# Optimization experiments

Measured on AMD Instinct MI355X. Metric: run time of the kernel, lower is better.

Reference implementation:

```python
import jax, jax.numpy as jnp
import numpy as np

N = 50000
E = 800000
IN_DIM = 128
HID = 128
OUT = 4
EPS = 1e-5


def setup_inputs() -> dict:
    key = jax.random.key(0)
    ks = jax.random.split(key, 16)
    glorot = lambda k, i, o: jax.random.uniform(k, (i, o), jnp.float32, -1.0, 1.0) * jnp.sqrt(6.0 / (i + o))
    return {
        "x": jax.random.normal(ks[0], (N, IN_DIM), jnp.float32),
        "edge_index": jax.random.randint(ks[1], (2, E), 0, N, jnp.int64),
        # SAGEConv layer 0: lin_l (aggregated neighbors, with bias), lin_r (self, no bias)
        "W_l0": glorot(ks[2], IN_DIM, HID), "b_l0": jnp.zeros((HID,), jnp.float32),
        "W_r0": glorot(ks[3], IN_DIM, HID),
        # SAGEConv layer 1
        "W_l1": glorot(ks[4], HID, HID), "b_l1": jnp.zeros((HID,), jnp.float32),
        "W_r1": glorot(ks[5], HID, HID),
        # LayerNorms
        "g0": jnp.ones((HID,), jnp.float32), "beta0": jnp.zeros((HID,), jnp.float32),
        "g1": jnp.ones((HID,), jnp.float32), "beta1": jnp.zeros((HID,), jnp.float32),
        # head
        "W_h": glorot(ks[6], HID, OUT), "b_h": jnp.zeros((OUT,), jnp.float32),
    }


def _sage_conv(x, src, dst, deg_inv, W_l, b_l, W_r):
    # mean-aggregate source features at destination nodes, then project
    agg = jax.ops.segment_sum(x[src], dst, num_segments=N) * deg_inv  # [N, d]
    return agg @ W_l + b_l + x @ W_r


def _layer_norm(x, g, b):
    mu = jnp.mean(x, axis=-1, keepdims=True)
    var = jnp.mean(jnp.square(x - mu), axis=-1, keepdims=True)
    return (x - mu) * jax.lax.rsqrt(var + EPS) * g + b


def reference(x, edge_index, W_l0, b_l0, W_r0, W_l1, b_l1, W_r1, g0, beta0, g1, beta1, W_h, b_h):
    src, dst = edge_index[0], edge_index[1]
    deg = jax.ops.segment_sum(jnp.ones((E,), jnp.float32), dst, num_segments=N)
    deg_inv = (1.0 / jnp.maximum(deg, 1.0))[:, None]  # mean over empty neighborhood -> 0

    h = _sage_conv(x, src, dst, deg_inv, W_l0, b_l0, W_r0)
    h = jax.nn.relu(_layer_norm(h, g0, beta0))
    h = _sage_conv(h, src, dst, deg_inv, W_l1, b_l1, W_r1)
    h = jax.nn.relu(_layer_norm(h, g1, beta1))
    return h @ W_h + b_h  # [N, 4]
```

## Files before the change

### kernel.cpp

```cpp
#include <hip/hip_runtime.h>

#define NN 50000
#define EE 800000
#define DIM 128
#define KK 256
#define OUTD 4
#define EPSV 1e-5f
#define OTS 132
#define NB 196
#define SLOT 8192
#define ACHUNK 4096
#define NA 196

using short8v = __attribute__((ext_vector_type(8))) short;
using f32x4v  = __attribute__((ext_vector_type(4))) float;

__device__ __forceinline__ unsigned short f2bf(float f) {
    union { float f; unsigned u; } x; x.f = f;
    unsigned r = x.u + 0x7FFF + ((x.u >> 16) & 1);
    return (unsigned short)(r >> 16);
}
__device__ __forceinline__ float bf2f(unsigned short u) {
    union { unsigned u; float f; } x; x.u = ((unsigned)u) << 16;
    return x.f;
}


#define XB_BLK 6250
#define W_BLK  256
__global__ __launch_bounds__(256) void prepA_kernel(
    const float* __restrict__ x, ushort* __restrict__ xqb,
    const float* __restrict__ Wl0, const float* __restrict__ Wr0,
    const float* __restrict__ Wl1, const float* __restrict__ Wr1,
    ushort* __restrict__ Wt0, ushort* __restrict__ Wt1,
    const int* __restrict__ src, const int* __restrict__ dst,
    int* __restrict__ bucketCursor, unsigned* __restrict__ pairs)
{
    int b = blockIdx.x;
    int tid = threadIdx.x;
    if (b < XB_BLK) {
        int i = b * 256 + tid;
        float4 v = ((const float4*)x)[i];
        ushort4 o;
        o.x = f2bf(v.x); o.y = f2bf(v.y); o.z = f2bf(v.z); o.w = f2bf(v.w);
        int node = i >> 5;
        int k = (i * 4) & 127;
        int p = k >> 5, off = k & 31;
        *(ushort4*)(xqb + ((size_t)p * NN + node) * 32 + off) = o;
        return;
    }
    if (b < XB_BLK + W_BLK) {
        int idx = (b - XB_BLK) * 256 + tid;
        int which = idx >> 15;
        int j = (idx >> 8) & 127;
        int k = idx & 255;
        const float* Wl = which ? Wl1 : Wl0;
        const float* Wr = which ? Wr1 : Wr0;
        ushort* Wt = which ? Wt1 : Wt0;
        float v = (k < 128) ? Wl[k * DIM + j] : Wr[(k - 128) * DIM + j];
        Wt[j * KK + k] = f2bf(v);
        return;
    }

    __shared__ int hist[256];
    __shared__ int scanb[256];
    __shared__ int exStart[256];
    __shared__ int cur2[256];
    __shared__ int gBase[256];
    __shared__ unsigned stage[ACHUNK];
    int ab = b - XB_BLK - W_BLK;
    int eBase = ab * ACHUNK;
    int total = min(ACHUNK, EE - eBase);

    hist[tid] = 0;
    __syncthreads();

    #pragma unroll
    for (int i = 0; i < 16; i++) {
        int idx = i * 256 + tid;
        if (idx < total) {
            int d = dst[eBase + idx];
            atomicAdd(&hist[d >> 8], 1);
        }
    }
    __syncthreads();
    int cntv = hist[tid];
    scanb[tid] = cntv;
    __syncthreads();
    #pragma unroll
    for (int off = 1; off < 256; off <<= 1) {
        int add = (tid >= off) ? scanb[tid - off] : 0;
        __syncthreads();
        scanb[tid] += add;
        __syncthreads();
    }
    int ex = scanb[tid] - cntv;
    exStart[tid] = ex;
    cur2[tid] = ex;
    if (tid < NB) gBase[tid] = (cntv > 0) ? atomicAdd(&bucketCursor[tid], cntv) : 0;
    __syncthreads();

    #pragma unroll
    for (int i = 0; i < 16; i++) {
        int idx = i * 256 + tid;
        if (idx < total) {
            int e = eBase + idx;
            int d = dst[e], s = src[e];
            int bb = d >> 8;
            int sp = atomicAdd(&cur2[bb], 1);
            stage[sp] = ((unsigned)d << 16) | (unsigned)s;
        }
    }
    __syncthreads();

    #pragma unroll
    for (int i = 0; i < 16; i++) {
        int idx = i * 256 + tid;
        if (idx < total) {
            unsigned v = stage[idx];
            int bb = v >> 24;
            int pos = gBase[bb] + (idx - exStart[bb]);
            if (pos < SLOT) pairs[(size_t)bb * SLOT + pos] = v;
        }
    }
}

__global__ __launch_bounds__(256) void passB_kernel(
    const int* __restrict__ bucketCursor,
    const unsigned* __restrict__ pairs,
    int* __restrict__ rowptr, ushort* __restrict__ colS)
{
    __shared__ int bscan[256];
    __shared__ int cw[256];
    __shared__ int pre2[256];
    __shared__ unsigned val_lds[SLOT];
    int tid = threadIdx.x;
    int b = blockIdx.x;

    int c = (tid < NB) ? min(bucketCursor[tid], SLOT) : 0;
    bscan[tid] = c;
    __syncthreads();
    #pragma unroll
    for (int off = 1; off < 256; off <<= 1) {
        int add = (tid >= off) ? bscan[tid - off] : 0;
        __syncthreads();
        bscan[tid] += add;
        __syncthreads();
    }
    int myBase = b ? bscan[b - 1] : 0;
    int count  = bscan[b] - myBase;
    __syncthreads();

    cw[tid] = 0;
    __syncthreads();

    const unsigned* pb = pairs + (size_t)b * SLOT;
    for (int p = tid; p < count; p += 256) {
        unsigned v = pb[p];
        val_lds[p] = v;
        atomicAdd(&cw[(v >> 16) & 255], 1);
    }
    __syncthreads();
    int cnode = cw[tid];
    bscan[tid] = cnode;
    __syncthreads();
    #pragma unroll
    for (int off = 1; off < 256; off <<= 1) {
        int add = (tid >= off) ? bscan[tid - off] : 0;
        __syncthreads();
        bscan[tid] += add;
        __syncthreads();
    }
    int preEx = bscan[tid] - cnode;
    pre2[tid] = preEx;
    int nodeBase = b << 8;
    if (nodeBase + tid < NN) rowptr[nodeBase + tid] = myBase + preEx;
    if (b == NB - 1 && tid == 0) rowptr[NN] = myBase + count;
    cw[tid] = 0;
    __syncthreads();

    for (int p = tid; p < count; p += 256) {
        unsigned v = val_lds[p];
        int dl = (v >> 16) & 255;
        int r = atomicAdd(&cw[dl], 1);
        colS[myBase + pre2[dl] + r] = (ushort)(v & 0xFFFF);
    }
}

template <int DO_HEAD>
__global__ __launch_bounds__(256) void sage_fused_kernel(
    const ushort* __restrict__ featG,
    const int* __restrict__ rowptr, const ushort* __restrict__ colS,
    const ushort* __restrict__ WtB,
    const float* __restrict__ bl,
    const float* __restrict__ g, const float* __restrict__ beta,
    const float* __restrict__ Wh, const float* __restrict__ bh,
    void* __restrict__ outp)
{
    __shared__ __align__(16) char smem[32 * OTS * 4];
    __shared__ float mu_s[32], ri_s[32];
    ushort* featB = (ushort*)smem;
    float*  oT    = (float*)smem;
    #define OT(n, k) oT[(n) * OTS + (k)]

    int tid = threadIdx.x;
    int base = blockIdx.x * 32;
    int lane = tid & 63, w = tid >> 6;

    #pragma unroll
    for (int i = 0; i < 2; i++) {
        int idx = tid + i * 256;
        int n = idx >> 4, c = idx & 15;
        int node = base + n;
        short8v xv = {};
        if (node < NN) {
            int p = c >> 2;
            int off = (c & 3) * 8;
            xv = *(const short8v*)(featG + ((size_t)p * NN + node) * 32 + off);
        }
        int kb = (256 + c * 16) ^ ((n & 7) << 4);
        *(short8v*)(featB + n * KK + (kb >> 1)) = xv;
    }

    {
        int n = tid >> 3;
        int sub = tid & 7;
        int node = base + n;
        int beg = 0, end = 0;
        if (node < NN) { beg = rowptr[node]; end = rowptr[node + 1]; }
        float di = 1.0f / fmaxf((float)(end - beg), 1.0f);
        #pragma unroll 1
        for (int p = 0; p < 4; p++) {
            const ushort* xq = featG + (size_t)p * NN * 32 + sub * 4;
            float a0[4], a1[4], a2[4], a3[4];
            #pragma unroll
            for (int j = 0; j < 4; j++) { a0[j] = 0.f; a1[j] = 0.f; a2[j] = 0.f; a3[j] = 0.f; }
            int e = beg;
            for (; e + 3 < end; e += 4) {
                int s0 = colS[e], s1 = colS[e + 1], s2 = colS[e + 2], s3 = colS[e + 3];
                ushort4 v0 = *(const ushort4*)(xq + s0 * 32);
                ushort4 v1 = *(const ushort4*)(xq + s1 * 32);
                ushort4 v2 = *(const ushort4*)(xq + s2 * 32);
                ushort4 v3 = *(const ushort4*)(xq + s3 * 32);
                a0[0] += bf2f(v0.x); a0[1] += bf2f(v0.y); a0[2] += bf2f(v0.z); a0[3] += bf2f(v0.w);
                a1[0] += bf2f(v1.x); a1[1] += bf2f(v1.y); a1[2] += bf2f(v1.z); a1[3] += bf2f(v1.w);
                a2[0] += bf2f(v2.x); a2[1] += bf2f(v2.y); a2[2] += bf2f(v2.z); a2[3] += bf2f(v2.w);
                a3[0] += bf2f(v3.x); a3[1] += bf2f(v3.y); a3[2] += bf2f(v3.z); a3[3] += bf2f(v3.w);
            }
            for (; e < end; e++) {
                int s0 = colS[e];
                ushort4 v0 = *(const ushort4*)(xq + s0 * 32);
                a0[0] += bf2f(v0.x); a0[1] += bf2f(v0.y); a0[2] += bf2f(v0.z); a0[3] += bf2f(v0.w);
            }
            ushort4 o;
            float r0 = (a0[0] + a1[0] + a2[0] + a3[0]) * di;
            float r1 = (a0[1] + a1[1] + a2[1] + a3[1]) * di;
            float r2 = (a0[2] + a1[2] + a2[2] + a3[2]) * di;
            float r3 = (a0[3] + a1[3] + a2[3] + a3[3]) * di;
            o.x = f2bf(r0); o.y = f2bf(r1); o.z = f2bf(r2); o.w = f2bf(r3);
            int kb = (p * 64 + sub * 8) ^ ((n & 7) << 4);
            *(ushort4*)(featB + n * KK + (kb >> 1)) = o;
        }
    }
    __syncthreads();

    int l15 = lane & 15, q = lane >> 4;
    f32x4v acc00 = {}, acc01 = {}, acc10 = {}, acc11 = {};
    const ushort* wbase = WtB + (size_t)(w * 32) * KK;
    int n0 = l15, n1 = 16 + l15;
    int sw = (l15 & 7) << 4;
    #pragma unroll
    for (int ks = 0; ks < 8; ks++) {
        int kbA = ks * 64 + q * 16;
        short8v a0 = *(const short8v*)(featB + n0 * KK + (((kbA) ^ sw) >> 1));
        short8v a1 = *(const short8v*)(featB + n1 * KK + (((kbA) ^ sw) >> 1));
        int koff = ks * 32 + q * 8;
        short8v b0 = *(const short8v*)(wbase + (size_t)l15 * KK + koff);
        short8v b1 = *(const short8v*)(wbase + (size_t)(16 + l15) * KK + koff);
        acc00 = __builtin_amdgcn_mfma_f32_16x16x32_bf16(a0, b0, acc00, 0, 0, 0);
        acc01 = __builtin_amdgcn_mfma_f32_16x16x32_bf16(a0, b1, acc01, 0, 0, 0);
        acc10 = __builtin_amdgcn_mfma_f32_16x16x32_bf16(a1, b0, acc10, 0, 0, 0);
        acc11 = __builtin_amdgcn_mfma_f32_16x16x32_bf16(a1, b1, acc11, 0, 0, 0);
    }
    __syncthreads();

    {
        int c0 = w * 32 + l15, c1 = c0 + 16;
        float bl0v = bl[c0], bl1v = bl[c1];
        #pragma unroll
        for (int r = 0; r < 4; r++) {
            int r0 = q * 4 + r, r1 = 16 + q * 4 + r;
            OT(r0, c0) = acc00[r] + bl0v;
            OT(r0, c1) = acc01[r] + bl1v;
            OT(r1, c0) = acc10[r] + bl0v;
            OT(r1, c1) = acc11[r] + bl1v;
        }
    }
    __syncthreads();

    {
        int n = tid >> 3, l = tid & 7;
        float s = 0.f, s2 = 0.f;
        #pragma unroll
        for (int kk = 0; kk < 16; kk++) {
            float v = OT(n, l * 16 + kk);
            s += v; s2 += v * v;
        }
        #pragma unroll
        for (int off = 4; off; off >>= 1) {
            s  += __shfl_down(s, off, 8);
            s2 += __shfl_down(s2, off, 8);
        }
        if (l == 0) {
            float mu = s * (1.0f / DIM);
            float var = s2 * (1.0f / DIM) - mu * mu;
            mu_s[n] = mu;
            ri_s[n] = rsqrtf(fmaxf(var, 0.f) + EPSV);
        }
    }
    __syncthreads();

    if (!DO_HEAD) {
        ushort* hout = (ushort*)outp;
        #pragma unroll
        for (int i = 0; i < 16; i++) {
            int idx = tid + i * 256;
            int n = idx >> 7, k = idx & 127;
            int node = base + n;
            if (node < NN) {
                float v = (OT(n, k) - mu_s[n]) * ri_s[n] * g[k] + beta[k];
                hout[((size_t)(k >> 5) * NN + node) * 32 + (k & 31)] = f2bf(fmaxf(v, 0.f));
            }
        }
    } else {
        float* fout = (float*)outp;
        float vals[16];
        #pragma unroll
        for (int i = 0; i < 16; i++) {
            int idx = tid + i * 256;
            int n = idx >> 7, k = idx & 127;
            float v = (OT(n, k) - mu_s[n]) * ri_s[n] * g[k] + beta[k];
            vals[i] = fmaxf(v, 0.f);
        }
        __syncthreads();
        #pragma unroll
        for (int i = 0; i < 16; i++) {
            int idx = tid + i * 256;
            int n = idx >> 7, k = idx & 127;
            OT(n, k) = vals[i];
        }
        __syncthreads();
        if (tid < 128) {
            int n = tid >> 2, o = tid & 3;
            int node = base + n;
            if (node < NN) {
                float s = bh[o];
                for (int k = 0; k < DIM; k++) s += OT(n, k) * Wh[k * OUTD + o];
                fout[(size_t)node * OUTD + o] = s;
            }
        }
    }
    #undef OT
}

extern "C" void kernel_launch(void* const* d_in, const int* in_sizes, int n_in,
                              void* d_out, int out_size, void* d_ws, size_t ws_size,
                              hipStream_t stream)
{
    const float* x    = (const float*)d_in[0];
    const int*   ei   = (const int*)d_in[1];
    const float* Wl0  = (const float*)d_in[2];
    const float* bl0  = (const float*)d_in[3];
    const float* Wr0  = (const float*)d_in[4];
    const float* Wl1  = (const float*)d_in[5];
    const float* bl1  = (const float*)d_in[6];
    const float* Wr1  = (const float*)d_in[7];
    const float* g0   = (const float*)d_in[8];
    const float* be0  = (const float*)d_in[9];
    const float* g1   = (const float*)d_in[10];
    const float* be1  = (const float*)d_in[11];
    const float* Wh   = (const float*)d_in[12];
    const float* bh   = (const float*)d_in[13];
    float* out = (float*)d_out;

    const int* srcI = ei;
    const int* dstI = ei + EE;

    char* p = (char*)d_ws;
    ushort*   xqb    = (ushort*)p;    p += (size_t)NN * DIM * 2;
    ushort*   h      = (ushort*)p;    p += (size_t)NN * DIM * 2;
    ushort*   Wt0    = (ushort*)p;    p += DIM * KK * 2;
    ushort*   Wt1    = (ushort*)p;    p += DIM * KK * 2;
    int*      rowptr = (int*)p;       p += 50016 * 4;
    int*      bucketCursor = (int*)p; p += 256 * 4;
    unsigned* pairs  = (unsigned*)p;  p += (size_t)NB * SLOT * 4;
    ushort*   colS   = (ushort*)p;    p += (size_t)EE * 2;

    hipMemsetAsync(bucketCursor, 0, 256 * sizeof(int), stream);
    prepA_kernel<<<XB_BLK + W_BLK + NA, 256, 0, stream>>>(
        x, xqb, Wl0, Wr0, Wl1, Wr1, Wt0, Wt1, srcI, dstI, bucketCursor, pairs);
    passB_kernel<<<NB, 256, 0, stream>>>(bucketCursor, pairs, rowptr, colS);

    const int blocks = (NN + 31) / 32;
    sage_fused_kernel<0><<<blocks, 256, 0, stream>>>(
        xqb, rowptr, colS, Wt0, bl0, g0, be0, nullptr, nullptr, (void*)h);
    sage_fused_kernel<1><<<blocks, 256, 0, stream>>>(
        h, rowptr, colS, Wt1, bl1, g1, be1, Wh, bh, (void*)out);
}
```

Baseline: 263.7 us.

## Stage block edge indices in LDS and gather with 16-byte vector loads

Before aggregation, each block copies the column indices for its 32 destination nodes into shared memory, so the neighbor loop reads indices from LDS instead of global memory. The gather is restructured so that each thread loads 8 bf16 features (16 bytes) per edge. Adjacent thread pairs split the edges by parity and combine their sums with a shuffle, where before each thread loaded 4 features. A fallback path reads indices from global memory when a block has more edges than the LDS capacity. The cost is an extra block-wide barrier and 4 KB of additional LDS per block, which may reduce occupancy.

```diff
diff --git a/kernel.cpp b/kernel.cpp
--- a/kernel.cpp
+++ b/kernel.cpp
@@ -11,6 +11,7 @@
 #define SLOT 8192
 #define ACHUNK 4096
 #define NA 196
+#define ECAP 2048
 
 using short8v = __attribute__((ext_vector_type(8))) short;
 using f32x4v  = __attribute__((ext_vector_type(4))) float;
@@ -199,6 +200,7 @@
 {
     __shared__ __align__(16) char smem[32 * OTS * 4];
     __shared__ float mu_s[32], ri_s[32];
+    __shared__ ushort colLds[ECAP];
     ushort* featB = (ushort*)smem;
     float*  oT    = (float*)smem;
     #define OT(n, k) oT[(n) * OTS + (k)]
@@ -206,6 +208,11 @@
     int tid = threadIdx.x;
     int base = blockIdx.x * 32;
     int lane = tid & 63, w = tid >> 6;
+
+    int beg0 = rowptr[base];
+    int end0 = rowptr[min(base + 32, NN)];
+    int cnt = end0 - beg0;
+    for (int i = tid; i < cnt && i < ECAP; i += 256) colLds[i] = colS[beg0 + i];
 
     #pragma unroll
     for (int i = 0; i < 2; i++) {
@@ -221,45 +228,81 @@
         int kb = (256 + c * 16) ^ ((n & 7) << 4);
         *(short8v*)(featB + n * KK + (kb >> 1)) = xv;
     }
+    __syncthreads();
 
     {
         int n = tid >> 3;
         int sub = tid & 7;
+        int chunk = sub >> 1;
+        int par = sub & 1;
         int node = base + n;
-        int beg = 0, end = 0;
-        if (node < NN) { beg = rowptr[node]; end = rowptr[node + 1]; }
-        float di = 1.0f / fmaxf((float)(end - beg), 1.0f);
-        #pragma unroll 1
-        for (int p = 0; p < 4; p++) {
-            const ushort* xq = featG + (size_t)p * NN * 32 + sub * 4;
-            float a0[4], a1[4], a2[4], a3[4];
-            #pragma unroll
-            for (int j = 0; j < 4; j++) { a0[j] = 0.f; a1[j] = 0.f; a2[j] = 0.f; a3[j] = 0.f; }
-            int e = beg;
-            for (; e + 3 < end; e += 4) {
-                int s0 = colS[e], s1 = colS[e + 1], s2 = colS[e + 2], s3 = colS[e + 3];
-                ushort4 v0 = *(const ushort4*)(xq + s0 * 32);
-                ushort4 v1 = *(const ushort4*)(xq + s1 * 32);
-                ushort4 v2 = *(const ushort4*)(xq + s2 * 32);
-                ushort4 v3 = *(const ushort4*)(xq + s3 * 32);
-                a0[0] += bf2f(v0.x); a0[1] += bf2f(v0.y); a0[2] += bf2f(v0.z); a0[3] += bf2f(v0.w);
-                a1[0] += bf2f(v1.x); a1[1] += bf2f(v1.y); a1[2] += bf2f(v1.z); a1[3] += bf2f(v1.w);
-                a2[0] += bf2f(v2.x); a2[1] += bf2f(v2.y); a2[2] += bf2f(v2.z); a2[3] += bf2f(v2.w);
-                a3[0] += bf2f(v3.x); a3[1] += bf2f(v3.y); a3[2] += bf2f(v3.z); a3[3] += bf2f(v3.w);
+        int nb = 0, ne = 0;
+        if (node < NN) { nb = rowptr[node]; ne = rowptr[node + 1]; }
+        float di = 1.0f / fmaxf((float)(ne - nb), 1.0f);
+        int sw = (n & 7) << 4;
+
+        if (cnt <= ECAP) {
+            int begL = nb - beg0, endL = ne - beg0;
+            #pragma unroll 1
+            for (int p = 0; p < 4; p++) {
+                const ushort* xq = featG + (size_t)p * NN * 32 + chunk * 8;
+                float a0[8], a1[8];
+                #pragma unroll
+                for (int j = 0; j < 8; j++) { a0[j] = 0.f; a1[j] = 0.f; }
+                int e = begL + par;
+                for (; e + 2 < endL; e += 4) {
+                    int s0 = colLds[e], s1 = colLds[e + 2];
+                    short8v v0 = *(const short8v*)(xq + (size_t)s0 * 32);
+                    short8v v1 = *(const short8v*)(xq + (size_t)s1 * 32);
+                    #pragma unroll
+                    for (int j = 0; j < 8; j++) {
+                        a0[j] += bf2f((unsigned short)v0[j]);
+                        a1[j] += bf2f((unsigned short)v1[j]);
+                    }
+                }
+                if (e < endL) {
+                    int s0 = colLds[e];
+                    short8v v0 = *(const short8v*)(xq + (size_t)s0 * 32);
+                    #pragma unroll
+                    for (int j = 0; j < 8; j++) a0[j] += bf2f((unsigned short)v0[j]);
+                }
+                short8v o;
+                #pragma unroll
+                for (int j = 0; j < 8; j++) {
+                    float t = a0[j] + a1[j];
+                    t += __shfl_xor(t, 1, 64);
+                    o[j] = (short)f2bf(t * di);
+                }
+                if (par == 0) {
+                    int kb = (p * 64 + chunk * 16) ^ sw;
+                    *(short8v*)(featB + n * KK + (kb >> 1)) = o;
+                }
             }
-            for (; e < end; e++) {
-                int s0 = colS[e];
-                ushort4 v0 = *(const ushort4*)(xq + s0 * 32);
-                a0[0] += bf2f(v0.x); a0[1] += bf2f(v0.y); a0[2] += bf2f(v0.z); a0[3] += bf2f(v0.w);
+        } else {
+            #pragma unroll 1
+            for (int p = 0; p < 4; p++) {
+                const ushort* xq = featG + (size_t)p * NN * 32 + chunk * 8;
+                float a[8];
+                #pragma unroll
+                for (int j = 0; j < 8; j++) a[j] = 0.f;
+                for (int e = nb + par; e < ne; e += 2) {
+                    int s0 = colS[e];
+                    short8v v0 = *(const short8v*)(xq + (size_t)s0 * 32);
+                    #pragma unroll
+                    for (int j = 0; j < 8; j++) a[j] += bf2f((unsigned short)v0[j]);
+                }
+                short8v o;
+                #pragma unroll
+                for (int j = 0; j < 8; j++) {
+                    float t = a[j];
+                    t += __shfl_xor(t, 1, 64);
+                    o[j] = (short)f2bf(t * di);
+                }
+                if (par == 0) {
+                    int kb = (p * 64 + chunk * 16) ^ sw;
+                    *(short8v*)(featB + n * KK + (kb >> 1)) = o;
+                }
             }
-            ushort4 o;
-            float r0 = (a0[0] + a1[0] + a2[0] + a3[0]) * di;
-            float r1 = (a0[1] + a1[1] + a2[1] + a3[1]) * di;
-            float r2 = (a0[2] + a1[2] + a2[2] + a3[2]) * di;
-            float r3 = (a0[3] + a1[3] + a2[3] + a3[3]) * di;
-            o.x = f2bf(r0); o.y = f2bf(r1); o.z = f2bf(r2); o.w = f2bf(r3);
-            int kb = (p * 64 + sub * 8) ^ ((n & 7) << 4);
-            *(ushort4*)(featB + n * KK + (kb >> 1)) = o;
         }
     }
     __syncthreads();
@@ -268,12 +311,12 @@
     f32x4v acc00 = {}, acc01 = {}, acc10 = {}, acc11 = {};
     const ushort* wbase = WtB + (size_t)(w * 32) * KK;
     int n0 = l15, n1 = 16 + l15;
-    int sw = (l15 & 7) << 4;
+    int sw2 = (l15 & 7) << 4;
     #pragma unroll
     for (int ks = 0; ks < 8; ks++) {
         int kbA = ks * 64 + q * 16;
-        short8v a0 = *(const short8v*)(featB + n0 * KK + (((kbA) ^ sw) >> 1));
-        short8v a1 = *(const short8v*)(featB + n1 * KK + (((kbA) ^ sw) >> 1));
+        short8v a0 = *(const short8v*)(featB + n0 * KK + (((kbA) ^ sw2) >> 1));
+        short8v a1 = *(const short8v*)(featB + n1 * KK + (((kbA) ^ sw2) >> 1));
         int koff = ks * 32 + q * 8;
         short8v b0 = *(const short8v*)(wbase + (size_t)l15 * KK + koff);
         short8v b1 = *(const short8v*)(wbase + (size_t)(16 + l15) * KK + koff);
```

After: 214.8 us. 1.23x faster.
